# Kernel optimization log

Hardware: AMD Instinct MI355X
Metric: run time of the kernel (lower is better)

Reference implementation:

```python
import jax, jax.numpy as jnp
import numpy as np

D_MODEL, D_STATE, D_CONV, EXPAND, DT_RANK = 1024, 16, 4, 2, 64
D_INNER = EXPAND * D_MODEL
B, L = 2, 4096


def setup_inputs() -> dict:
    key = jax.random.key(0)
    ks = jax.random.split(key, 9)
    s = 0.02
    x = jax.random.normal(ks[0], (B, L, D_MODEL), dtype=jnp.float32)
    in_proj_w = jax.random.normal(ks[1], (D_MODEL, 2 * D_INNER), dtype=jnp.float32) * s
    conv_w = jax.random.normal(ks[2], (D_INNER, 1, D_CONV), dtype=jnp.float32) * s
    conv_b = jnp.zeros((D_INNER,), dtype=jnp.float32)
    x_proj_w = jax.random.normal(ks[3], (D_INNER, DT_RANK + 2 * D_STATE), dtype=jnp.float32) * s
    dt_proj_w = jax.random.normal(ks[4], (DT_RANK, D_INNER), dtype=jnp.float32) * s
    # dt bias -> softplus(dt) roughly in [1e-3, 1e-1] as in mamba init
    dt = jnp.exp(jax.random.uniform(ks[5], (D_INNER,)) * (np.log(0.1) - np.log(1e-3)) + np.log(1e-3))
    dt_proj_b = (dt + jnp.log(-jnp.expm1(-dt))).astype(jnp.float32)  # inverse softplus
    A_log = jnp.log(jnp.broadcast_to(jnp.arange(1, D_STATE + 1, dtype=jnp.float32), (D_INNER, D_STATE)))
    Dp = jnp.ones((D_INNER,), dtype=jnp.float32)
    out_proj_w = jax.random.normal(ks[6], (D_INNER, D_MODEL), dtype=jnp.float32) * s
    return {"x": x, "in_proj_w": in_proj_w, "conv_w": conv_w, "conv_b": conv_b,
            "x_proj_w": x_proj_w, "dt_proj_w": dt_proj_w, "dt_proj_b": dt_proj_b,
            "A_log": A_log, "Dp": Dp, "out_proj_w": out_proj_w}


def _mamba(x, in_proj_w, conv_w, conv_b, x_proj_w, dt_proj_w, dt_proj_b, A_log, Dp, out_proj_w):
    # in projection -> (u, z), each [B, L, D_INNER]
    xz = jnp.einsum('bld,de->ble', x, in_proj_w)
    u, z = jnp.split(xz, 2, axis=-1)
    # causal depthwise conv1d over time
    u_c = jax.lax.conv_general_dilated(
        u.transpose(0, 2, 1), conv_w, window_strides=(1,),
        padding=[(D_CONV - 1, 0)],
        dimension_numbers=('NCH', 'OIH', 'NCH'),
        feature_group_count=D_INNER)
    u_c = jax.nn.silu(u_c.transpose(0, 2, 1) + conv_b)  # [B, L, D_INNER]
    # input-dependent dt, B, C
    dbc = jnp.einsum('bld,dr->blr', u_c, x_proj_w)
    dt_lo, Bc, Cc = jnp.split(dbc, [DT_RANK, DT_RANK + D_STATE], axis=-1)
    dt = jax.nn.softplus(jnp.einsum('blr,rd->bld', dt_lo, dt_proj_w) + dt_proj_b)  # [B,L,Di]
    A = -jnp.exp(A_log)  # [Di, N]

    def step(h, inp):
        u_t, dt_t, B_t, C_t = inp  # [B,Di],[B,Di],[B,N],[B,N]
        dA = jnp.exp(dt_t[..., None] * A)                      # [B,Di,N]
        h = h * dA + (dt_t * u_t)[..., None] * B_t[:, None, :]  # [B,Di,N]
        y = jnp.einsum('bdn,bn->bd', h, C_t)                   # [B,Di]
        return h, y

    h0 = jnp.zeros((x.shape[0], D_INNER, D_STATE), dtype=x.dtype)
    xs = (u_c.transpose(1, 0, 2), dt.transpose(1, 0, 2),
          Bc.transpose(1, 0, 2), Cc.transpose(1, 0, 2))
    _, ys = jax.lax.scan(step, h0, xs)      # [L, B, Di]
    y = ys.transpose(1, 0, 2) + u_c * Dp    # skip connection
    y = y * jax.nn.silu(z)                  # gate
    return jnp.einsum('bld,de->ble', y, out_proj_w)


def reference(x, in_proj_w, conv_w, conv_b, x_proj_w, dt_proj_w, dt_proj_b, A_log, Dp, out_proj_w):
    return _mamba(x, in_proj_w, conv_w, conv_b, x_proj_w, dt_proj_w, dt_proj_b, A_log, Dp, out_proj_w)
```

## Files before the change

kernel.cpp:

```cpp
#include <hip/hip_runtime.h>
#include <hip/hip_bf16.h>
#include <math.h>

#define BSZ 2
#define LSEQ 4096
#define DMODEL 1024
#define DINNER 2048
#define NSTATE 16
#define DTRANK 64
#define MROWS (BSZ * LSEQ)
#define NCHUNK 64
#define CHUNK (LSEQ / NCHUNK)
#define XKS 8
#define XKCH (DINNER / XKS)

#if __has_builtin(__builtin_amdgcn_exp2f)
#define EXP2F(x) __builtin_amdgcn_exp2f(x)
#else
#define EXP2F(x) exp2f(x)
#endif
#define LOG2E 1.44269504088896f

typedef __attribute__((ext_vector_type(8))) short bf16x8;
typedef __attribute__((ext_vector_type(4))) float f32x4;

__device__ __forceinline__ float sigmoidf_(float x) { return 1.0f / (1.0f + __expf(-x)); }

__device__ __forceinline__ unsigned short f2bf(float x) {
    unsigned int u = __float_as_uint(x);
    u += 0x7fff + ((u >> 16) & 1);
    return (unsigned short)(u >> 16);
}
__device__ __forceinline__ float bf2f(unsigned short b) {
    return __uint_as_float(((unsigned int)b) << 16);
}

__global__ __launch_bounds__(256) void prep_kernel(
    const float* __restrict__ x, unsigned short* __restrict__ xbf,
    const float* __restrict__ w_in, unsigned short* __restrict__ wT_in,
    const float* __restrict__ w_out, unsigned short* __restrict__ wT_out,
    const float* __restrict__ w_x, unsigned short* __restrict__ wXT,
    const float* __restrict__ w_dt, unsigned short* __restrict__ wDT)
{
    __shared__ float tile[64][65];
    const int id = blockIdx.x;
    const int t = threadIdx.x;

    if (id >= 1632) {
        int gid = (id - 1632) * 256 + t;
        int m = gid >> 7;
        int g = gid & 127;
        size_t src = (size_t)m * 1024 + g * 8;
        float4 v0 = *reinterpret_cast<const float4*>(x + src);
        float4 v1 = *reinterpret_cast<const float4*>(x + src + 4);
        uint4 w;
        w.x = (unsigned)f2bf(v0.x) | ((unsigned)f2bf(v0.y) << 16);
        w.y = (unsigned)f2bf(v0.z) | ((unsigned)f2bf(v0.w) << 16);
        w.z = (unsigned)f2bf(v1.x) | ((unsigned)f2bf(v1.y) << 16);
        w.w = (unsigned)f2bf(v1.z) | ((unsigned)f2bf(v1.w) << 16);
        size_t dst = (size_t)m * 1024 + ((g * 8) ^ ((m & 7) << 3));
        *reinterpret_cast<uint4*>(xbf + dst) = w;
        return;
    }

    const float* W; unsigned short* WT; int K, Nsrc, nb, kb;
    if (id < 1024)      { W = w_in;  WT = wT_in;  K = 1024; Nsrc = 4096; nb = id & 63; kb = id >> 6; }
    else if (id < 1536) { int q = id - 1024; W = w_out; WT = wT_out; K = 2048; Nsrc = 1024; nb = q & 15; kb = q >> 4; }
    else if (id < 1600) { int q = id - 1536; W = w_x;   WT = wXT;   K = 2048; Nsrc = 96;   nb = q & 1;  kb = q >> 1; }
    else                { int q = id - 1600; W = w_dt;  WT = wDT;   K = 64;   Nsrc = 2048; nb = q;      kb = 0; }

    const int n0 = nb * 64;
    const int k0 = kb * 64;

    #pragma unroll
    for (int i = 0; i < 16; ++i) {
        int flat = i * 256 + t;
        int r = flat >> 6, c = flat & 63;
        tile[r][c] = (n0 + c < Nsrc) ? W[(size_t)(k0 + r) * Nsrc + n0 + c] : 0.0f;
    }
    __syncthreads();
    #pragma unroll
    for (int i = 0; i < 16; ++i) {
        int flat = i * 256 + t;
        int n = flat >> 6, k = flat & 63;
        int ks = k ^ ((n & 7) << 3);
        WT[(size_t)(n0 + n) * K + k0 + ks] = f2bf(tile[k][n]);
    }
}

template<int OBF>
__global__ __launch_bounds__(256) void gemm_bb_kernel(
    const unsigned short* __restrict__ Abf, const unsigned short* __restrict__ BT,
    void* __restrict__ Cv, int M, int N, int K, int ldc)
{
    __shared__ unsigned short lds_a[128 * 64];
    __shared__ unsigned short lds_b[128 * 64];

    const int nwg = gridDim.x * gridDim.y;
    const int wg  = blockIdx.y * gridDim.x + blockIdx.x;
    const int cpx = nwg >> 3;
    const int swz = (wg & 7) * cpx + (wg >> 3);
    const int bx  = swz % gridDim.x;
    const int by  = swz / gridDim.x;

    const int tid  = threadIdx.x;
    const int lane = tid & 63;
    const int w    = tid >> 6;
    const int wr   = (w >> 1) * 64;
    const int wc   = (w & 1) * 64;
    const int row0 = by * 128;
    const int col0 = bx * 128;

    f32x4 acc[4][4];
    #pragma unroll
    for (int m = 0; m < 4; ++m)
        #pragma unroll
        for (int n = 0; n < 4; ++n)
            acc[m][n] = (f32x4){0.f, 0.f, 0.f, 0.f};

    for (int k0 = 0; k0 < K; k0 += 64) {
        #pragma unroll
        for (int j = 0; j < 4; ++j) {
            int c  = (j * 4 + w) * 64 + lane;
            int r  = c >> 3;
            int cc = c & 7;
            const char* asrc = (const char*)Abf +
                ((size_t)(row0 + r) * K + k0) * 2 + cc * 16;
            __builtin_amdgcn_global_load_lds(
                (const __attribute__((address_space(1))) void*)asrc,
                (__attribute__((address_space(3))) void*)((char*)lds_a + (j * 4 + w) * 1024),
                16, 0, 0);
            const char* bsrc = (const char*)BT +
                ((size_t)(col0 + r) * K + k0) * 2 + cc * 16;
            __builtin_amdgcn_global_load_lds(
                (const __attribute__((address_space(1))) void*)bsrc,
                (__attribute__((address_space(3))) void*)((char*)lds_b + (j * 4 + w) * 1024),
                16, 0, 0);
        }
        __syncthreads();

        #pragma unroll
        for (int kk = 0; kk < 2; ++kk) {
            bf16x8 af[4], bfr[4];
            #pragma unroll
            for (int m = 0; m < 4; ++m) {
                int r = wr + m * 16 + (lane & 15);
                int byteoff = r * 128 + ((kk * 64 + (lane >> 4) * 16) ^ ((r & 7) << 4));
                af[m] = *reinterpret_cast<const bf16x8*>((const char*)lds_a + byteoff);
            }
            #pragma unroll
            for (int n = 0; n < 4; ++n) {
                int r = wc + n * 16 + (lane & 15);
                int byteoff = r * 128 + ((kk * 64 + (lane >> 4) * 16) ^ ((r & 7) << 4));
                bfr[n] = *reinterpret_cast<const bf16x8*>((const char*)lds_b + byteoff);
            }
            #pragma unroll
            for (int m = 0; m < 4; ++m)
                #pragma unroll
                for (int n = 0; n < 4; ++n)
                    acc[m][n] = __builtin_amdgcn_mfma_f32_16x16x32_bf16(
                        af[m], bfr[n], acc[m][n], 0, 0, 0);
        }
        __syncthreads();
    }

    #pragma unroll
    for (int m = 0; m < 4; ++m) {
        int rbase = row0 + wr + m * 16 + (lane >> 4) * 4;
        #pragma unroll
        for (int n = 0; n < 4; ++n) {
            int col = col0 + wc + n * 16 + (lane & 15);
            #pragma unroll
            for (int r = 0; r < 4; ++r) {
                if (OBF) {
                    ((unsigned short*)Cv)[(size_t)(rbase + r) * ldc + col] =
                        f2bf(acc[m][n][r]);
                } else {
                    ((float*)Cv)[(size_t)(rbase + r) * ldc + col] = acc[m][n][r];
                }
            }
        }
    }
}

__global__ __launch_bounds__(256) void xproj_splitk_bb_kernel(
    const unsigned short* __restrict__ Abf, const unsigned short* __restrict__ BT,
    float* __restrict__ part)
{
    __shared__ unsigned short lds_a[128 * 64];
    __shared__ unsigned short lds_b[128 * 64];

    const int tid  = threadIdx.x;
    const int lane = tid & 63;
    const int w    = tid >> 6;
    const int wr   = (w >> 1) * 64;
    const int wc   = (w & 1) * 64;
    const int row0 = blockIdx.y * 128;
    const int kb   = blockIdx.z * XKCH;
    const int K    = DINNER;

    f32x4 acc[4][4];
    #pragma unroll
    for (int m = 0; m < 4; ++m)
        #pragma unroll
        for (int n = 0; n < 4; ++n)
            acc[m][n] = (f32x4){0.f, 0.f, 0.f, 0.f};

    for (int k0 = kb; k0 < kb + XKCH; k0 += 64) {
        #pragma unroll
        for (int j = 0; j < 4; ++j) {
            int c  = (j * 4 + w) * 64 + lane;
            int r  = c >> 3;
            int cc = c & 7;
            const char* asrc = (const char*)Abf +
                ((size_t)(row0 + r) * K + k0) * 2 + cc * 16;
            __builtin_amdgcn_global_load_lds(
                (const __attribute__((address_space(1))) void*)asrc,
                (__attribute__((address_space(3))) void*)((char*)lds_a + (j * 4 + w) * 1024),
                16, 0, 0);
            const char* bsrc = (const char*)BT +
                ((size_t)r * K + k0) * 2 + cc * 16;
            __builtin_amdgcn_global_load_lds(
                (const __attribute__((address_space(1))) void*)bsrc,
                (__attribute__((address_space(3))) void*)((char*)lds_b + (j * 4 + w) * 1024),
                16, 0, 0);
        }
        __syncthreads();

        #pragma unroll
        for (int kk = 0; kk < 2; ++kk) {
            bf16x8 af[4], bfr[4];
            #pragma unroll
            for (int m = 0; m < 4; ++m) {
                int r = wr + m * 16 + (lane & 15);
                int byteoff = r * 128 + ((kk * 64 + (lane >> 4) * 16) ^ ((r & 7) << 4));
                af[m] = *reinterpret_cast<const bf16x8*>((const char*)lds_a + byteoff);
            }
            #pragma unroll
            for (int n = 0; n < 4; ++n) {
                int r = wc + n * 16 + (lane & 15);
                int byteoff = r * 128 + ((kk * 64 + (lane >> 4) * 16) ^ ((r & 7) << 4));
                bfr[n] = *reinterpret_cast<const bf16x8*>((const char*)lds_b + byteoff);
            }
            #pragma unroll
            for (int m = 0; m < 4; ++m)
                #pragma unroll
                for (int n = 0; n < 4; ++n)
                    acc[m][n] = __builtin_amdgcn_mfma_f32_16x16x32_bf16(
                        af[m], bfr[n], acc[m][n], 0, 0, 0);
        }
        __syncthreads();
    }

    float* pbase = part + (size_t)blockIdx.z * MROWS * 96;
    #pragma unroll
    for (int m = 0; m < 4; ++m) {
        int rbase = row0 + wr + m * 16 + (lane >> 4) * 4;
        #pragma unroll
        for (int n = 0; n < 4; ++n) {
            int col = wc + n * 16 + (lane & 15);
            if (col < 96) {
                #pragma unroll
                for (int r = 0; r < 4; ++r)
                    pbase[(size_t)(rbase + r) * 96 + col] = acc[m][n][r];
            }
        }
    }
}

__global__ __launch_bounds__(256) void xproj_reduce_kernel(
    const float* __restrict__ part, float* __restrict__ dbc,
    unsigned short* __restrict__ dtlo)
{
    int gid = blockIdx.x * 256 + threadIdx.x;
    float s = 0.f;
    #pragma unroll
    for (int k = 0; k < XKS; ++k)
        s += part[(size_t)k * MROWS * 96 + gid];
    dbc[gid] = s;
    int row = gid / 96;
    int col = gid - row * 96;
    if (col < 64)
        dtlo[(size_t)row * 64 + (col ^ ((row & 7) << 3))] = f2bf(s);
}

__global__ __launch_bounds__(256) void gemm_dtproj_bb_kernel(
    const unsigned short* __restrict__ Abf, const unsigned short* __restrict__ BT,
    const float* __restrict__ bias, unsigned short* __restrict__ C)
{
    __shared__ unsigned short lds_a[128 * 64];
    __shared__ unsigned short lds_b[128 * 64];

    const int tid  = threadIdx.x;
    const int lane = tid & 63;
    const int w    = tid >> 6;
    const int wr   = (w >> 1) * 64;
    const int wc   = (w & 1) * 64;
    const int row0 = blockIdx.y * 128;
    const int col0 = blockIdx.x * 128;

    f32x4 acc[4][4];
    #pragma unroll
    for (int m = 0; m < 4; ++m)
        #pragma unroll
        for (int n = 0; n < 4; ++n)
            acc[m][n] = (f32x4){0.f, 0.f, 0.f, 0.f};

    #pragma unroll
    for (int j = 0; j < 4; ++j) {
        int c  = (j * 4 + w) * 64 + lane;
        int r  = c >> 3;
        int cc = c & 7;
        const char* asrc = (const char*)Abf + ((size_t)(row0 + r) * 64) * 2 + cc * 16;
        __builtin_amdgcn_global_load_lds(
            (const __attribute__((address_space(1))) void*)asrc,
            (__attribute__((address_space(3))) void*)((char*)lds_a + (j * 4 + w) * 1024),
            16, 0, 0);
        const char* bsrc = (const char*)BT + ((size_t)(col0 + r) * 64) * 2 + cc * 16;
        __builtin_amdgcn_global_load_lds(
            (const __attribute__((address_space(1))) void*)bsrc,
            (__attribute__((address_space(3))) void*)((char*)lds_b + (j * 4 + w) * 1024),
            16, 0, 0);
    }
    __syncthreads();

    #pragma unroll
    for (int kk = 0; kk < 2; ++kk) {
        bf16x8 af[4], bfr[4];
        #pragma unroll
        for (int m = 0; m < 4; ++m) {
            int r = wr + m * 16 + (lane & 15);
            int byteoff = r * 128 + ((kk * 64 + (lane >> 4) * 16) ^ ((r & 7) << 4));
            af[m] = *reinterpret_cast<const bf16x8*>((const char*)lds_a + byteoff);
        }
        #pragma unroll
        for (int n = 0; n < 4; ++n) {
            int r = wc + n * 16 + (lane & 15);
            int byteoff = r * 128 + ((kk * 64 + (lane >> 4) * 16) ^ ((r & 7) << 4));
            bfr[n] = *reinterpret_cast<const bf16x8*>((const char*)lds_b + byteoff);
        }
        #pragma unroll
        for (int m = 0; m < 4; ++m)
            #pragma unroll
            for (int n = 0; n < 4; ++n)
                acc[m][n] = __builtin_amdgcn_mfma_f32_16x16x32_bf16(
                    af[m], bfr[n], acc[m][n], 0, 0, 0);
    }

    #pragma unroll
    for (int m = 0; m < 4; ++m) {
        int rbase = row0 + wr + m * 16 + (lane >> 4) * 4;
        #pragma unroll
        for (int n = 0; n < 4; ++n) {
            int col = col0 + wc + n * 16 + (lane & 15);
            float bv = bias[col];
            #pragma unroll
            for (int r = 0; r < 4; ++r) {
                float v = acc[m][n][r] + bv;
                v = (v > 20.0f) ? v : log1pf(__expf(v));
                C[(size_t)(rbase + r) * DINNER + col] = f2bf(v);
            }
        }
    }
}

__global__ __launch_bounds__(256) void conv_silu_kernel(
    const unsigned short* __restrict__ xzb, const float* __restrict__ cw,
    const float* __restrict__ cb, unsigned short* __restrict__ ucbf)
{
    int gid = blockIdx.x * 256 + threadIdx.x;
    int row = gid >> 8;
    int d0  = (gid & 255) * 8;
    int t = row & (LSEQ - 1);

    uint4 uv[4];
    #pragma unroll
    for (int k = 0; k < 4; ++k) {
        if (t - 3 + k >= 0)
            uv[k] = *reinterpret_cast<const uint4*>(
                xzb + (size_t)(row + k - 3) * 4096 + d0);
        else
            uv[k] = (uint4){0u, 0u, 0u, 0u};
    }

    float v[8];
    #pragma unroll
    for (int i = 0; i < 8; ++i) {
        float acc = cb[d0 + i];
        float4 wv = *reinterpret_cast<const float4*>(cw + (size_t)(d0 + i) * 4);
        float wk[4] = {wv.x, wv.y, wv.z, wv.w};
        #pragma unroll
        for (int k = 0; k < 4; ++k) {
            unsigned int word = (&uv[k].x)[i >> 1];
            float u = __uint_as_float((i & 1) ? (word & 0xffff0000u) : (word << 16));
            acc = fmaf(u, wk[k], acc);
        }
        v[i] = acc * sigmoidf_(acc);
    }

    uint4 o;
    o.x = (unsigned)f2bf(v[0]) | ((unsigned)f2bf(v[1]) << 16);
    o.y = (unsigned)f2bf(v[2]) | ((unsigned)f2bf(v[3]) << 16);
    o.z = (unsigned)f2bf(v[4]) | ((unsigned)f2bf(v[5]) << 16);
    o.w = (unsigned)f2bf(v[6]) | ((unsigned)f2bf(v[7]) << 16);
    *reinterpret_cast<uint4*>(
        ucbf + (size_t)row * DINNER + (d0 ^ ((row & 7) << 3))) = o;
}

__global__ __launch_bounds__(256) void scan_partial_kernel(
    const unsigned short* __restrict__ dtb, const unsigned short* __restrict__ ucbf,
    const float* __restrict__ dbc, const float* __restrict__ A_log,
    float* __restrict__ Pbuf, float* __restrict__ Ebuf)
{
    __shared__ float sB[CHUNK][NSTATE];
    const int tid = threadIdx.x;
    const int c = blockIdx.x;
    const int b = blockIdx.z;
    const int d = blockIdx.y * 256 + tid;
    const size_t row0 = (size_t)b * LSEQ + c * CHUNK;

    {
        int s = tid >> 2, f = tid & 3;
        float4 v = *reinterpret_cast<const float4*>(dbc + (row0 + s) * 96 + 64 + f * 4);
        *reinterpret_cast<float4*>(&sB[s][f * 4]) = v;
    }

    float An2[NSTATE];
    #pragma unroll
    for (int k = 0; k < 4; ++k) {
        float4 a = *reinterpret_cast<const float4*>(A_log + (size_t)d * NSTATE + k * 4);
        An2[k*4+0] = -__expf(a.x) * LOG2E;
        An2[k*4+1] = -__expf(a.y) * LOG2E;
        An2[k*4+2] = -__expf(a.z) * LOG2E;
        An2[k*4+3] = -__expf(a.w) * LOG2E;
    }
    __syncthreads();

    float E[NSTATE];
    #pragma unroll
    for (int n = 0; n < NSTATE; ++n) E[n] = 0.f;
    float S = 0.f;

    float dtc = bf2f(dtb[row0 * DINNER + d]);
    float ucv = bf2f(ucbf[row0 * DINNER + d]);
    for (int s = 0; s < CHUNK; ++s) {
        float dtn = 0.f, un = 0.f;
        if (s + 1 < CHUNK) {
            dtn = bf2f(dtb[(row0 + s + 1) * DINNER + d]);
            un  = bf2f(ucbf[(row0 + s + 1) * DINNER + (d ^ (((s + 1) & 7) << 3))]);
        }
        S += dtc;
        float du = dtc * ucv;
        float Bv[NSTATE];
        #pragma unroll
        for (int k = 0; k < 4; ++k)
            *reinterpret_cast<float4*>(&Bv[k*4]) =
                *reinterpret_cast<const float4*>(&sB[s][k*4]);
        #pragma unroll
        for (int n = 0; n < NSTATE; ++n) {
            float q = EXP2F(dtc * An2[n]);
            E[n] = fmaf(E[n], q, du * Bv[n]);
        }
        dtc = dtn; ucv = un;
    }

    size_t base = (((size_t)c * BSZ + b) * DINNER + d) * NSTATE;
    #pragma unroll
    for (int n = 0; n < NSTATE; ++n) {
        Pbuf[base + n] = EXP2F(An2[n] * S);
        Ebuf[base + n] = E[n];
    }
}

__global__ __launch_bounds__(256) void scan_prefix_kernel(
    float* __restrict__ Pbuf, const float* __restrict__ Ebuf)
{
    const int gid = blockIdx.x * 256 + threadIdx.x;
    const size_t stride = (size_t)BSZ * DINNER * NSTATE;
    size_t idx = gid;
    float h = 0.f;
    for (int c = 0; c < NCHUNK; ++c) {
        float P = Pbuf[idx];
        float Ev = Ebuf[idx];
        Pbuf[idx] = h;
        h = fmaf(P, h, Ev);
        idx += stride;
    }
}

__global__ __launch_bounds__(256) void scan_final_kernel(
    const unsigned short* __restrict__ dtb, const unsigned short* __restrict__ ucbf,
    const unsigned short* __restrict__ xzb, const float* __restrict__ dbc,
    const float* __restrict__ A_log, const float* __restrict__ Dp,
    const float* __restrict__ H0, unsigned short* __restrict__ ybf)
{
    __shared__ float sBC[CHUNK][2 * NSTATE];
    const int tid = threadIdx.x;
    const int c = blockIdx.x;
    const int b = blockIdx.z;
    const int d = blockIdx.y * 256 + tid;
    const size_t row0 = (size_t)b * LSEQ + c * CHUNK;

    {
        #pragma unroll
        for (int i = 0; i < 2; ++i) {
            int j = tid * 2 + i;
            int s = j >> 3, f = j & 7;
            float4 v = *reinterpret_cast<const float4*>(dbc + (row0 + s) * 96 + 64 + f * 4);
            *reinterpret_cast<float4*>(&sBC[s][f * 4]) = v;
        }
    }

    float An2[NSTATE];
    #pragma unroll
    for (int k = 0; k < 4; ++k) {
        float4 a = *reinterpret_cast<const float4*>(A_log + (size_t)d * NSTATE + k * 4);
        An2[k*4+0] = -__expf(a.x) * LOG2E;
        An2[k*4+1] = -__expf(a.y) * LOG2E;
        An2[k*4+2] = -__expf(a.z) * LOG2E;
        An2[k*4+3] = -__expf(a.w) * LOG2E;
    }
    const float Dpd = Dp[d];

    float h[NSTATE];
    {
        size_t base = (((size_t)c * BSZ + b) * DINNER + d) * NSTATE;
        #pragma unroll
        for (int n = 0; n < NSTATE; ++n) h[n] = H0[base + n];
    }
    __syncthreads();

    float dtc = bf2f(dtb[row0 * DINNER + d]);
    float ucv = bf2f(ucbf[row0 * DINNER + d]);
    float zc  = bf2f(xzb[row0 * 4096 + 2048 + d]);
    for (int s = 0; s < CHUNK; ++s) {
        float dtn = 0.f, un = 0.f, zn = 0.f;
        if (s + 1 < CHUNK) {
            dtn = bf2f(dtb[(row0 + s + 1) * DINNER + d]);
            un  = bf2f(ucbf[(row0 + s + 1) * DINNER + (d ^ (((s + 1) & 7) << 3))]);
            zn  = bf2f(xzb[(row0 + s + 1) * 4096 + 2048 + d]);
        }
        float du = dtc * ucv;
        float Bv[NSTATE], Cv[NSTATE];
        #pragma unroll
        for (int k = 0; k < 4; ++k) {
            *reinterpret_cast<float4*>(&Bv[k*4]) =
                *reinterpret_cast<const float4*>(&sBC[s][k*4]);
            *reinterpret_cast<float4*>(&Cv[k*4]) =
                *reinterpret_cast<const float4*>(&sBC[s][16 + k*4]);
        }
        float y0 = 0.f, y1 = 0.f, y2 = 0.f, y3 = 0.f;
        #pragma unroll
        for (int n = 0; n < NSTATE; ++n) {
            float q = EXP2F(dtc * An2[n]);
            h[n] = fmaf(h[n], q, du * Bv[n]);
            float& yk = (n & 3) == 0 ? y0 : (n & 3) == 1 ? y1 : (n & 3) == 2 ? y2 : y3;
            yk = fmaf(h[n], Cv[n], yk);
        }
        float y = (y0 + y1) + (y2 + y3);
        float yg = (y + ucv * Dpd) * (zc * sigmoidf_(zc));
        ybf[(row0 + s) * DINNER + (d ^ ((s & 7) << 3))] = f2bf(yg);
        dtc = dtn; ucv = un; zc = zn;
    }
}

extern "C" void kernel_launch(void* const* d_in, const int* in_sizes, int n_in,
                              void* d_out, int out_size, void* d_ws, size_t ws_size,
                              hipStream_t stream)
{
    const float* x         = (const float*)d_in[0];
    const float* in_proj_w = (const float*)d_in[1];
    const float* conv_w    = (const float*)d_in[2];
    const float* conv_b    = (const float*)d_in[3];
    const float* x_proj_w  = (const float*)d_in[4];
    const float* dt_proj_w = (const float*)d_in[5];
    const float* dt_proj_b = (const float*)d_in[6];
    const float* A_log     = (const float*)d_in[7];
    const float* Dp        = (const float*)d_in[8];
    const float* out_proj_w= (const float*)d_in[9];
    float* out = (float*)d_out;

    char* base = (char*)d_ws;
    unsigned short* xzb  = (unsigned short*)base;
    unsigned short* dtb  = (unsigned short*)(base + (64ull << 20));
    unsigned short* ucbf = (unsigned short*)(base + (96ull << 20));
    float* dbc           = (float*)(base + (128ull << 20));
    unsigned short* wT_in  = (unsigned short*)(base + (131ull << 20));
    unsigned short* wT_out = (unsigned short*)(base + (139ull << 20));
    unsigned short* wXT    = (unsigned short*)(base + (143ull << 20));
    unsigned short* wDT    = (unsigned short*)(base + (143ull << 20) + (512ull << 10));
    char* U = base + (144ull << 20);
    unsigned short* xbf  = (unsigned short*)U;
    float* part          = (float*)U;
    unsigned short* dtlo = (unsigned short*)(U + (24ull << 20));
    float* Pbuf          = (float*)U;
    float* Ebuf          = (float*)(U + (16ull << 20));
    unsigned short* ybf  = (unsigned short*)(U + (32ull << 20));

    dim3 blk(256);

    prep_kernel<<<dim3(5728), blk, 0, stream>>>(
        x, xbf, in_proj_w, wT_in, out_proj_w, wT_out, x_proj_w, wXT, dt_proj_w, wDT);

    gemm_bb_kernel<1><<<dim3(32, 64), blk, 0, stream>>>(
        xbf, wT_in, (void*)xzb, MROWS, 4096, 1024, 4096);

    conv_silu_kernel<<<dim3((MROWS * (DINNER / 8)) / 256), blk, 0, stream>>>(
        xzb, conv_w, conv_b, ucbf);

    xproj_splitk_bb_kernel<<<dim3(1, 64, XKS), blk, 0, stream>>>(ucbf, wXT, part);
    xproj_reduce_kernel<<<dim3((MROWS * 96) / 256), blk, 0, stream>>>(part, dbc, dtlo);

    gemm_dtproj_bb_kernel<<<dim3(16, 64), blk, 0, stream>>>(dtlo, wDT, dt_proj_b, dtb);

    scan_partial_kernel<<<dim3(NCHUNK, DINNER / 256, BSZ), blk, 0, stream>>>(
        dtb, ucbf, dbc, A_log, Pbuf, Ebuf);
    scan_prefix_kernel<<<dim3((BSZ * DINNER * NSTATE) / 256), blk, 0, stream>>>(Pbuf, Ebuf);
    scan_final_kernel<<<dim3(NCHUNK, DINNER / 256, BSZ), blk, 0, stream>>>(
        dtb, ucbf, xzb, dbc, A_log, Dp, Pbuf, ybf);

    gemm_bb_kernel<0><<<dim3(8, 64), blk, 0, stream>>>(
        ybf, wT_out, (void*)out, MROWS, 1024, 2048, 1024);
}
```

Measured before the change: 403.9 us.

## Double-buffer LDS tiles in bf16 GEMM kernels to overlap loads with MFMA

```diff
diff --git a/kernel.cpp b/kernel.cpp
--- a/kernel.cpp
+++ b/kernel.cpp
@@ -93,23 +93,17 @@
     const unsigned short* __restrict__ Abf, const unsigned short* __restrict__ BT,
     void* __restrict__ Cv, int M, int N, int K, int ldc)
 {
-    __shared__ unsigned short lds_a[128 * 64];
-    __shared__ unsigned short lds_b[128 * 64];
-
-    const int nwg = gridDim.x * gridDim.y;
-    const int wg  = blockIdx.y * gridDim.x + blockIdx.x;
-    const int cpx = nwg >> 3;
-    const int swz = (wg & 7) * cpx + (wg >> 3);
-    const int bx  = swz % gridDim.x;
-    const int by  = swz / gridDim.x;
+    __shared__ unsigned short lds_a[2][128 * 64];
+    __shared__ unsigned short lds_b[2][128 * 64];
 
     const int tid  = threadIdx.x;
     const int lane = tid & 63;
     const int w    = tid >> 6;
     const int wr   = (w >> 1) * 64;
     const int wc   = (w & 1) * 64;
-    const int row0 = by * 128;
-    const int col0 = bx * 128;
+    const int row0 = blockIdx.y * 128;
+    const int col0 = blockIdx.x * 128;
+    const int NT   = K >> 6;
 
     f32x4 acc[4][4];
     #pragma unroll
@@ -118,26 +112,36 @@
         for (int n = 0; n < 4; ++n)
             acc[m][n] = (f32x4){0.f, 0.f, 0.f, 0.f};
 
-    for (int k0 = 0; k0 < K; k0 += 64) {
+    auto STAGE = [&](int bi, int kt) {
+        int k0 = kt << 6;
         #pragma unroll
         for (int j = 0; j < 4; ++j) {
             int c  = (j * 4 + w) * 64 + lane;
             int r  = c >> 3;
             int cc = c & 7;
-            const char* asrc = (const char*)Abf +
-                ((size_t)(row0 + r) * K + k0) * 2 + cc * 16;
             __builtin_amdgcn_global_load_lds(
-                (const __attribute__((address_space(1))) void*)asrc,
-                (__attribute__((address_space(3))) void*)((char*)lds_a + (j * 4 + w) * 1024),
-                16, 0, 0);
-            const char* bsrc = (const char*)BT +
-                ((size_t)(col0 + r) * K + k0) * 2 + cc * 16;
+                (const __attribute__((address_space(1))) void*)
+                    ((const char*)Abf + ((size_t)(row0 + r) * K + k0) * 2 + cc * 16),
+                (__attribute__((address_space(3))) void*)
+                    ((char*)lds_a[bi] + (j * 4 + w) * 1024), 16, 0, 0);
             __builtin_amdgcn_global_load_lds(
-                (const __attribute__((address_space(1))) void*)bsrc,
-                (__attribute__((address_space(3))) void*)((char*)lds_b + (j * 4 + w) * 1024),
-                16, 0, 0);
-        }
-        __syncthreads();
+                (const __attribute__((address_space(1))) void*)
+                    ((const char*)BT + ((size_t)(col0 + r) * K + k0) * 2 + cc * 16),
+                (__attribute__((address_space(3))) void*)
+                    ((char*)lds_b[bi] + (j * 4 + w) * 1024), 16, 0, 0);
+        }
+    };
+
+    STAGE(0, 0);
+    for (int t = 0; t < NT; ++t) {
+        const int cur = t & 1;
+        if (t + 1 < NT) {
+            STAGE(cur ^ 1, t + 1);
+            asm volatile("s_waitcnt vmcnt(8)" ::: "memory");
+        } else {
+            asm volatile("s_waitcnt vmcnt(0)" ::: "memory");
+        }
+        __builtin_amdgcn_s_barrier();
 
         #pragma unroll
         for (int kk = 0; kk < 2; ++kk) {
@@ -146,13 +150,13 @@
             for (int m = 0; m < 4; ++m) {
                 int r = wr + m * 16 + (lane & 15);
                 int byteoff = r * 128 + ((kk * 64 + (lane >> 4) * 16) ^ ((r & 7) << 4));
-                af[m] = *reinterpret_cast<const bf16x8*>((const char*)lds_a + byteoff);
+                af[m] = *reinterpret_cast<const bf16x8*>((const char*)lds_a[cur] + byteoff);
             }
             #pragma unroll
             for (int n = 0; n < 4; ++n) {
                 int r = wc + n * 16 + (lane & 15);
                 int byteoff = r * 128 + ((kk * 64 + (lane >> 4) * 16) ^ ((r & 7) << 4));
-                bfr[n] = *reinterpret_cast<const bf16x8*>((const char*)lds_b + byteoff);
+                bfr[n] = *reinterpret_cast<const bf16x8*>((const char*)lds_b[cur] + byteoff);
             }
             #pragma unroll
             for (int m = 0; m < 4; ++m)
@@ -161,7 +165,8 @@
                     acc[m][n] = __builtin_amdgcn_mfma_f32_16x16x32_bf16(
                         af[m], bfr[n], acc[m][n], 0, 0, 0);
         }
-        __syncthreads();
+        asm volatile("s_waitcnt lgkmcnt(0)" ::: "memory");
+        __builtin_amdgcn_s_barrier();
     }
 
     #pragma unroll
@@ -187,8 +192,8 @@
     const unsigned short* __restrict__ Abf, const unsigned short* __restrict__ BT,
     float* __restrict__ part)
 {
-    __shared__ unsigned short lds_a[128 * 64];
-    __shared__ unsigned short lds_b[128 * 64];
+    __shared__ unsigned short lds_a[2][128 * 64];
+    __shared__ unsigned short lds_b[2][128 * 64];
 
     const int tid  = threadIdx.x;
     const int lane = tid & 63;
@@ -198,6 +203,7 @@
     const int row0 = blockIdx.y * 128;
     const int kb   = blockIdx.z * XKCH;
     const int K    = DINNER;
+    const int NT   = XKCH >> 6;
 
     f32x4 acc[4][4];
     #pragma unroll
@@ -206,26 +212,36 @@
         for (int n = 0; n < 4; ++n)
             acc[m][n] = (f32x4){0.f, 0.f, 0.f, 0.f};
 
-    for (int k0 = kb; k0 < kb + XKCH; k0 += 64) {
+    auto STAGE = [&](int bi, int kt) {
+        int k0 = kb + (kt << 6);
         #pragma unroll
         for (int j = 0; j < 4; ++j) {
             int c  = (j * 4 + w) * 64 + lane;
             int r  = c >> 3;
             int cc = c & 7;
-            const char* asrc = (const char*)Abf +
-                ((size_t)(row0 + r) * K + k0) * 2 + cc * 16;
             __builtin_amdgcn_global_load_lds(
-                (const __attribute__((address_space(1))) void*)asrc,
-                (__attribute__((address_space(3))) void*)((char*)lds_a + (j * 4 + w) * 1024),
-                16, 0, 0);
-            const char* bsrc = (const char*)BT +
-                ((size_t)r * K + k0) * 2 + cc * 16;
+                (const __attribute__((address_space(1))) void*)
+                    ((const char*)Abf + ((size_t)(row0 + r) * K + k0) * 2 + cc * 16),
+                (__attribute__((address_space(3))) void*)
+                    ((char*)lds_a[bi] + (j * 4 + w) * 1024), 16, 0, 0);
             __builtin_amdgcn_global_load_lds(
-                (const __attribute__((address_space(1))) void*)bsrc,
-                (__attribute__((address_space(3))) void*)((char*)lds_b + (j * 4 + w) * 1024),
-                16, 0, 0);
-        }
-        __syncthreads();
+                (const __attribute__((address_space(1))) void*)
+                    ((const char*)BT + ((size_t)r * K + k0) * 2 + cc * 16),
+                (__attribute__((address_space(3))) void*)
+                    ((char*)lds_b[bi] + (j * 4 + w) * 1024), 16, 0, 0);
+        }
+    };
+
+    STAGE(0, 0);
+    for (int t = 0; t < NT; ++t) {
+        const int cur = t & 1;
+        if (t + 1 < NT) {
+            STAGE(cur ^ 1, t + 1);
+            asm volatile("s_waitcnt vmcnt(8)" ::: "memory");
+        } else {
+            asm volatile("s_waitcnt vmcnt(0)" ::: "memory");
+        }
+        __builtin_amdgcn_s_barrier();
 
         #pragma unroll
         for (int kk = 0; kk < 2; ++kk) {
@@ -234,13 +250,13 @@
             for (int m = 0; m < 4; ++m) {
                 int r = wr + m * 16 + (lane & 15);
                 int byteoff = r * 128 + ((kk * 64 + (lane >> 4) * 16) ^ ((r & 7) << 4));
-                af[m] = *reinterpret_cast<const bf16x8*>((const char*)lds_a + byteoff);
+                af[m] = *reinterpret_cast<const bf16x8*>((const char*)lds_a[cur] + byteoff);
             }
             #pragma unroll
             for (int n = 0; n < 4; ++n) {
                 int r = wc + n * 16 + (lane & 15);
                 int byteoff = r * 128 + ((kk * 64 + (lane >> 4) * 16) ^ ((r & 7) << 4));
-                bfr[n] = *reinterpret_cast<const bf16x8*>((const char*)lds_b + byteoff);
+                bfr[n] = *reinterpret_cast<const bf16x8*>((const char*)lds_b[cur] + byteoff);
             }
             #pragma unroll
             for (int m = 0; m < 4; ++m)
@@ -249,7 +265,8 @@
                     acc[m][n] = __builtin_amdgcn_mfma_f32_16x16x32_bf16(
                         af[m], bfr[n], acc[m][n], 0, 0, 0);
         }
-        __syncthreads();
+        asm volatile("s_waitcnt lgkmcnt(0)" ::: "memory");
+        __builtin_amdgcn_s_barrier();
     }
 
     float* pbase = part + (size_t)blockIdx.z * MROWS * 96;
```

New measurement: 392.7 us. -2.8%, faster.
